# Kernel optimization log

Measured on AMD Instinct MI355X. Metric: run time of the kernel, lower is better.

## Reference

```python
import jax, jax.numpy as jnp
import numpy as np

# Spiking-neuron constants (ALIF_Neuron / output_Neuron are not in the given
# source; we use the standard surrogate-gradient spiking update from this repo
# family: mem = prev*decay*(1-spike) + input; spike = Heaviside(mem-thresh)).
THRESH = 0.5
LENS = 0.5
DECAY = 0.2

B, T, I, H = 64, 512, 256, 512

@jax.custom_vjp
def spike_fn(v):
    return (v > THRESH).astype(v.dtype)

def _spike_fwd(v):
    return spike_fn(v), v

def _spike_bwd(v, g):
    sg = (jnp.abs(v - THRESH) < LENS).astype(v.dtype) / (2.0 * LENS)
    return (g * sg,)

spike_fn.defvjp(_spike_fwd, _spike_bwd)


def setup_inputs() -> dict:
    key = jax.random.key(0)
    ks = jax.random.split(key, 7)
    sc = 0.05
    return {
        "x": jax.random.normal(ks[0], (B, T, I), jnp.float32),
        "Wx0": jax.random.normal(ks[1], (I, 4 * H), jnp.float32) * sc,
        "Wh0": jax.random.normal(ks[2], (H, 4 * H), jnp.float32) * sc,
        "bh0": jax.random.normal(ks[3], (4 * H,), jnp.float32) * sc,
        "Wx1": jax.random.normal(ks[4], (H, 4 * H), jnp.float32) * sc,
        "Wh1": jax.random.normal(ks[5], (H, 4 * H), jnp.float32) * sc,
        "bh1": jax.random.normal(ks[6], (4 * H,), jnp.float32) * sc,
    }


def _cell(xt, s, h, c, Wx, Wh, bh, is_output):
    # ifgo: [B, 4H]; chunk order i, f, g, o as in the torch code
    ifgo = xt @ Wx + h @ Wh + bh
    i, f, g, o = jnp.split(ifgo, 4, axis=-1)
    c_next = jax.nn.sigmoid(f) * c + jax.nn.sigmoid(i) * jnp.tanh(g)
    h_next = jax.nn.sigmoid(o) * jnp.tanh(c_next)
    if is_output:
        # output_Neuron(x, h_next): leaky integration of membrane with input
        h_next = h_next * DECAY + xt
        return s, h_next, c_next
    # ALIF_Neuron(s, h_next, s): adaptive mem update + surrogate spike
    mem = s * DECAY * (1.0 - s) + h_next
    s_new = spike_fn(mem)
    return s_new, mem, c_next


def reference(x, Wx0, Wh0, bh0, Wx1, Wh1, bh1):
    Bb = x.shape[0]
    z = jnp.zeros((Bb, H), x.dtype)
    init = (z, z, z, z, z, z)  # s0, h0, c0, s1, h1, c1

    def step(carry, xt):
        s0, h0, c0, s1, h1, c1 = carry
        s0, h0, c0 = _cell(xt, s0, h0, c0, Wx0, Wh0, bh0, False)
        # layer 1 consumes the spike output s0 of layer 0
        s1, h1, c1 = _cell(s0, s1, h1, c1, Wx1, Wh1, bh1, True)
        return (s0, h0, c0, s1, h1, c1), h1

    xs = jnp.swapaxes(x, 0, 1)  # [T, B, I]
    carry, outs = jax.lax.scan(step, init, xs)
    out = jnp.swapaxes(outs, 0, 1)  # [B, T, H] (batch_first)
    s0, h0, c0, s1, h1, c1 = carry
    s = jnp.stack([s0, s1])
    h = jnp.stack([h0, h1])
    c = jnp.stack([c0, c1])
    return out, s, h, c
```

## Files before the change

### kernel.cpp

```cpp
#include <hip/hip_runtime.h>
#include <math.h>

typedef float vf4 __attribute__((ext_vector_type(4)));

constexpr int T  = 512;
constexpr int BB = 64;
constexpr int II = 256;
constexpr int HH = 512;

constexpr int SOFF = BB * T * HH;
constexpr int HOFF = SOFF + 2 * BB * HH;
constexpr int COFF = HOFF + 2 * BB * HH;

constexpr int WS_WC0 = 0;
constexpr int WS_WC1 = 1572864;
constexpr int WS_BH0 = 3670016;
constexpr int WS_BH1 = 3672064;
constexpr int WS_HX0 = 3674112;
constexpr int WS_HX1 = 3739648;

__device__ __forceinline__ void bypass_st(float* p, float v) {
  asm volatile("global_store_dword %0, %1, off sc1" :: "v"(p), "v"(v) : "memory");
}
__device__ __forceinline__ void bypass_ld2x4(const vf4* p0, const vf4* p1, vf4& r0, vf4& r1) {
  asm volatile(
      "global_load_dwordx4 %0, %2, off sc1\n\t"
      "global_load_dwordx4 %1, %3, off sc1\n\t"
      "s_waitcnt vmcnt(0)"
      : "=&v"(r0), "=&v"(r1) : "v"(p0), "v"(p1) : "memory");
}

__device__ __forceinline__ bool tag_ok(float v, bool hi) {
  return hi ? (v > 6.0f) : (v > 2.0f && v < 6.0f);
}

__device__ __forceinline__ float sigf(float x) { return 1.0f / (1.0f + __expf(-x)); }
__device__ __forceinline__ float tanh_fast(float x) {
  return 1.0f - 2.0f / (1.0f + __expf(2.0f * x));
}

__device__ __forceinline__ float sxor(float v, int m) { return __shfl_xor(v, m, 64); }
__device__ __forceinline__ vf4 sxor4(vf4 v, int m) {
  vf4 r; r.x = sxor(v.x, m); r.y = sxor(v.y, m); r.z = sxor(v.z, m); r.w = sxor(v.w, m);
  return r;
}

__device__ __forceinline__ int rev3(int v) {
  return ((v & 1) << 2) | (v & 2) | ((v >> 2) & 1);
}

__device__ __forceinline__ vf4 reduce8(const vf4* acc, int kl) {
  const int sel = kl & 1;
  vf4 n0[4];
#pragma unroll
  for (int i = 0; i < 4; ++i) {
    vf4 snd = sel ? acc[i] : acc[i + 4];
    vf4 kp  = sel ? acc[i + 4] : acc[i];
    n0[i] = kp + sxor4(snd, 1);
  }
  const int sel2 = (kl >> 1) & 1;
  vf4 n1[2];
#pragma unroll
  for (int i = 0; i < 2; ++i) {
    vf4 snd = sel2 ? n0[i] : n0[i + 2];
    vf4 kp  = sel2 ? n0[i + 2] : n0[i];
    n1[i] = kp + sxor4(snd, 2);
  }
  const int sel3 = (kl >> 2) & 1;
  vf4 snd = sel3 ? n1[0] : n1[1];
  vf4 kp  = sel3 ? n1[1] : n1[0];
  vf4 r = kp + sxor4(snd, 4);
  r += sxor4(r, 8);
  r += sxor4(r, 16);
  r += sxor4(r, 32);
  return r;
}

__global__ void pack_wc(const float* __restrict__ A, const float* __restrict__ B,
                        int Ka, int K, float* __restrict__ Wp) {
  const int j = blockIdx.x;
  for (int k = threadIdx.x; k < K; k += 256) {
    const float* src = (k < Ka) ? (A + (size_t)k * 2048) : (B + (size_t)(k - Ka) * 2048);
    vf4 v = {src[j], src[512 + j], src[1024 + j], src[1536 + j]};
    ((vf4*)Wp)[(size_t)j * K + k] = v;
  }
}

__global__ void pack_bias(const float* __restrict__ bh0, const float* __restrict__ bh1,
                          float* __restrict__ bh0p, float* __restrict__ bh1p) {
  const int i = blockIdx.x * blockDim.x + threadIdx.x;
  if (i < 2048) {
    bh0p[i] = bh0[(i & 3) * 512 + (i >> 2)];
  } else {
    int q = i - 2048;
    bh1p[q] = bh1[(q & 3) * 512 + (q >> 2)];
  }
}

__global__ void fill_tag(float* __restrict__ p, float v) {
  p[blockIdx.x * 1024 + threadIdx.x] = v;
}

__global__ __launch_bounds__(1024, 4) void aslstm_main(
    const vf4* __restrict__ Wc0p, const vf4* __restrict__ Wc1p,
    const vf4* __restrict__ bh0p, const vf4* __restrict__ bh1p,
    const float* __restrict__ x,
    float* __restrict__ hx0, float* __restrict__ hx1,
    float* __restrict__ out) {
  const int wg  = blockIdx.x;
  const int xcd = wg & 7;
  const int a   = wg >> 3;
  const int g   = a & 7;
  const int s   = (a >> 3) * 8 + xcd;
  const int tid = threadIdx.x;
  const int jo  = tid >> 6;
  const int kl  = tid & 63;
  const int j   = s * 16 + jo;
  const int b_loc  = rev3(kl & 7);
  const int b_glob = g * 8 + b_loc;
  const bool rep0  = (kl < 8);

  __shared__ float cat0[2][8][776];
  __shared__ float cat1[2][8][1032];

  float c0 = 0.0f, c1 = 0.0f, sp = 0.0f;

  const int pl = (jo << 1) | (kl >> 5);
  const int lc = kl & 31;
  const int js = pl * 16 + (lc >> 1);
  const int b0 = (lc & 1) * 4;
  const int fo = g * 4096 + pl * 128 + lc * 4;

  vf4 w0r[3][4];
  {
    const vf4* wr = Wc0p + (size_t)j * 768;
#pragma unroll
    for (int ig = 0; ig < 3; ++ig) {
      const int k0 = ig * 256 + kl * 4;
#pragma unroll
      for (int q = 0; q < 4; ++q) w0r[ig][q] = wr[k0 + q];
    }
  }

  if (tid < 512) {
    int bx = tid >> 6, kx = (tid & 63) * 4;
    *(vf4*)&cat0[0][bx][kx] = *(const vf4*)&x[(size_t)(g * 8 + bx) * (T * II) + kx];
  }
  {
    int bz = tid >> 7, kz = (tid & 127) * 4;
    *(vf4*)&cat0[0][bz][256 + kz] = vf4{0.0f, 0.0f, 0.0f, 0.0f};
  }
  __syncthreads();

  for (int t = 0; t < T; ++t) {
    const int p0 = t & 1, p1 = p0 ^ 1;
    const bool tagm = ((t >> 1) & 1) != 0;
    const bool tagh = (((t + 3) >> 1) & 1) != 0;
    const float offm = tagm ? 8.0f : 4.0f;
    const float offh = tagh ? 8.0f : 4.0f;

    vf4 acc[8];
#pragma unroll
    for (int b = 0; b < 8; ++b) acc[b] = vf4{0, 0, 0, 0};
#pragma unroll
    for (int ig = 0; ig < 3; ++ig) {
      const int k0 = ig * 256 + kl * 4;
#pragma unroll
      for (int b = 0; b < 8; ++b) {
        vf4 av = *(const vf4*)&cat0[p0][b][k0];
        acc[b] += av.x * w0r[ig][0]; acc[b] += av.y * w0r[ig][1];
        acc[b] += av.z * w0r[ig][2]; acc[b] += av.w * w0r[ig][3];
      }
    }

    {
      vf4 p = reduce8(acc, kl) + bh0p[j];
      float cn  = sigf(p.y) * c0 + sigf(p.x) * tanh_fast(p.z);
      float mem = sigf(p.w) * tanh_fast(cn);
      float sn  = (mem > 0.5f) ? 1.0f : 0.0f;
      c0 = cn; sp = sn;
      if (rep0) {
        bypass_st(&hx0[p0 * 32768 + g * 4096 + j * 8 + b_loc], mem + offm);
        if (t == T - 1) {
          out[SOFF + b_glob * 512 + j] = sn;
          out[HOFF + b_glob * 512 + j] = mem;
          out[COFF + b_glob * 512 + j] = cn;
        }
      }
    }

    vf4 xv = vf4{0, 0, 0, 0};
    if (tid < 512 && t < T - 1) {
      int bx = tid >> 6, kx = (tid & 63) * 4;
      xv = *(const vf4*)&x[(size_t)(g * 8 + bx) * (T * II) + (size_t)(t + 1) * II + kx];
    }

    {
      const vf4* mp = (const vf4*)(hx0 + p0 * 32768 + fo);
      const vf4* hp = (const vf4*)(hx1 + p1 * 32768 + fo);
      vf4 mv, hv;
      int tries = 0;
      for (;;) {
        bypass_ld2x4(mp, hp, mv, hv);
        bool ok = tag_ok(mv.x, tagm) && tag_ok(mv.y, tagm) &&
                  tag_ok(mv.z, tagm) && tag_ok(mv.w, tagm) &&
                  tag_ok(hv.x, tagh) && tag_ok(hv.y, tagh) &&
                  tag_ok(hv.z, tagh) && tag_ok(hv.w, tagh);
        if (__all(ok)) break;
        if (++tries > 4) __builtin_amdgcn_s_sleep(1);
      }
      const vf4 om = {offm, offm, offm, offm};
      const vf4 oh = {offh, offh, offh, offh};
      vf4 mm = mv - om;
      vf4 hh = hv - oh;
      cat0[p1][b0 + 0][256 + js] = mm.x;
      cat0[p1][b0 + 1][256 + js] = mm.y;
      cat0[p1][b0 + 2][256 + js] = mm.z;
      cat0[p1][b0 + 3][256 + js] = mm.w;
      cat1[p0][b0 + 0][js] = (mm.x > 0.5f) ? 1.0f : 0.0f;
      cat1[p0][b0 + 1][js] = (mm.y > 0.5f) ? 1.0f : 0.0f;
      cat1[p0][b0 + 2][js] = (mm.z > 0.5f) ? 1.0f : 0.0f;
      cat1[p0][b0 + 3][js] = (mm.w > 0.5f) ? 1.0f : 0.0f;
      cat1[p0][b0 + 0][512 + js] = hh.x;
      cat1[p0][b0 + 1][512 + js] = hh.y;
      cat1[p0][b0 + 2][512 + js] = hh.z;
      cat1[p0][b0 + 3][512 + js] = hh.w;
      if (tid < 512) {
        int bx = tid >> 6, kx = (tid & 63) * 4;
        *(vf4*)&cat0[p1][bx][kx] = xv;
      }
    }
    __syncthreads();

#pragma unroll
    for (int b = 0; b < 8; ++b) acc[b] = vf4{0, 0, 0, 0};
    {
      const vf4* wr = Wc1p + (size_t)j * 1024;
#pragma unroll
      for (int ig = 0; ig < 4; ++ig) {
        const int k0 = ig * 256 + kl * 4;
        vf4 w0 = wr[k0], w1 = wr[k0 + 1], w2 = wr[k0 + 2], w3 = wr[k0 + 3];
#pragma unroll
        for (int b = 0; b < 8; ++b) {
          vf4 av = *(const vf4*)&cat1[p0][b][k0];
          acc[b] += av.x * w0; acc[b] += av.y * w1;
          acc[b] += av.z * w2; acc[b] += av.w * w3;
        }
      }
    }

    {
      vf4 p = reduce8(acc, kl) + bh1p[j];
      float cn  = sigf(p.y) * c1 + sigf(p.x) * tanh_fast(p.z);
      float hn  = sigf(p.w) * tanh_fast(cn);
      float h1n = hn * 0.2f + sp;
      c1 = cn;
      if (rep0) {
        bypass_st(&hx1[p0 * 32768 + g * 4096 + j * 8 + b_loc], h1n + offm);
        out[(size_t)b_glob * (T * HH) + (size_t)t * HH + j] = h1n;
        if (t == T - 1) {
          out[HOFF + 32768 + b_glob * 512 + j] = h1n;
          out[COFF + 32768 + b_glob * 512 + j] = cn;
        }
      }
    }
  }
}

extern "C" void kernel_launch(void* const* d_in, const int* in_sizes, int n_in,
                              void* d_out, int out_size, void* d_ws, size_t ws_size,
                              hipStream_t stream) {
  const float* x   = (const float*)d_in[0];
  const float* Wx0 = (const float*)d_in[1];
  const float* Wh0 = (const float*)d_in[2];
  const float* bh0 = (const float*)d_in[3];
  const float* Wx1 = (const float*)d_in[4];
  const float* Wh1 = (const float*)d_in[5];
  const float* bh1 = (const float*)d_in[6];
  float* out = (float*)d_out;
  float* ws  = (float*)d_ws;

  float* Wc0p  = ws + WS_WC0;
  float* Wc1p  = ws + WS_WC1;
  float* bh0pf = ws + WS_BH0;
  float* bh1pf = ws + WS_BH1;
  float* hx0   = ws + WS_HX0;
  float* hx1   = ws + WS_HX1;

  hipMemsetAsync(hx0, 0, 2 * 64 * 512 * sizeof(float), stream);
  hipMemsetAsync(hx1, 0, 64 * 512 * sizeof(float), stream);
  hipMemsetAsync(out + SOFF + BB * HH, 0, BB * HH * sizeof(float), stream);

  pack_wc<<<dim3(512), dim3(256), 0, stream>>>(Wx0, Wh0, 256, 768, Wc0p);
  pack_wc<<<dim3(512), dim3(256), 0, stream>>>(Wx1, Wh1, 512, 1024, Wc1p);
  pack_bias<<<dim3(16), dim3(256), 0, stream>>>(bh0, bh1, bh0pf, bh1pf);
  fill_tag<<<dim3(32), dim3(1024), 0, stream>>>(hx1 + 32768, 8.0f);

  aslstm_main<<<dim3(256), dim3(1024), 0, stream>>>(
      (const vf4*)Wc0p, (const vf4*)Wc1p, (const vf4*)bh0pf, (const vf4*)bh1pf,
      x, hx0, hx1, out);
}
```

Before: 7.482 ms.

## Split recurrent LSTM blocks to 8 hidden units and drop LDS double buffering

The persistent recurrent kernel now launches 512 workgroups of 512 threads instead of 256 of 1024, so each workgroup owns 8 hidden units. The cross-workgroup exchange is widened: each thread polls and loads two 16-byte chunks per buffer and writes them straight into a single-buffered LDS layout. The LDS double buffers are removed and an extra barrier is added before the exchange writes. The polling backoff also gains a longer sleep tier. The aim is smaller, cheaper per-block barriers and more even spread across CUs, at the cost of twice as many workgroups polling the global flags and one more barrier per step.

```diff
diff --git a/kernel.cpp b/kernel.cpp
--- a/kernel.cpp
+++ b/kernel.cpp
@@ -22,16 +22,23 @@
 __device__ __forceinline__ void bypass_st(float* p, float v) {
   asm volatile("global_store_dword %0, %1, off sc1" :: "v"(p), "v"(v) : "memory");
 }
-__device__ __forceinline__ void bypass_ld2x4(const vf4* p0, const vf4* p1, vf4& r0, vf4& r1) {
+__device__ __forceinline__ void bypass_ld4x4(const vf4* p0, const vf4* p1,
+                                             vf4& m0, vf4& m1, vf4& h0, vf4& h1) {
   asm volatile(
-      "global_load_dwordx4 %0, %2, off sc1\n\t"
-      "global_load_dwordx4 %1, %3, off sc1\n\t"
+      "global_load_dwordx4 %0, %4, off sc1\n\t"
+      "global_load_dwordx4 %1, %4, off offset:16 sc1\n\t"
+      "global_load_dwordx4 %2, %5, off sc1\n\t"
+      "global_load_dwordx4 %3, %5, off offset:16 sc1\n\t"
       "s_waitcnt vmcnt(0)"
-      : "=&v"(r0), "=&v"(r1) : "v"(p0), "v"(p1) : "memory");
+      : "=&v"(m0), "=&v"(m1), "=&v"(h0), "=&v"(h1)
+      : "v"(p0), "v"(p1) : "memory");
 }
 
 __device__ __forceinline__ bool tag_ok(float v, bool hi) {
   return hi ? (v > 6.0f) : (v > 2.0f && v < 6.0f);
+}
+__device__ __forceinline__ bool tag_ok4(vf4 v, bool hi) {
+  return tag_ok(v.x, hi) && tag_ok(v.y, hi) && tag_ok(v.z, hi) && tag_ok(v.w, hi);
 }
 
 __device__ __forceinline__ float sigf(float x) { return 1.0f / (1.0f + __expf(-x)); }
@@ -101,7 +108,7 @@
   p[blockIdx.x * 1024 + threadIdx.x] = v;
 }
 
-__global__ __launch_bounds__(1024, 4) void aslstm_main(
+__global__ __launch_bounds__(512, 4) void aslstm_main(
     const vf4* __restrict__ Wc0p, const vf4* __restrict__ Wc1p,
     const vf4* __restrict__ bh0p, const vf4* __restrict__ bh1p,
     const float* __restrict__ x,
@@ -115,21 +122,17 @@
   const int tid = threadIdx.x;
   const int jo  = tid >> 6;
   const int kl  = tid & 63;
-  const int j   = s * 16 + jo;
+  const int j   = s * 8 + jo;
   const int b_loc  = rev3(kl & 7);
   const int b_glob = g * 8 + b_loc;
   const bool rep0  = (kl < 8);
 
-  __shared__ float cat0[2][8][776];
-  __shared__ float cat1[2][8][1032];
+  __shared__ float cat0[8][776];
+  __shared__ float cat1[8][1032];
 
   float c0 = 0.0f, c1 = 0.0f, sp = 0.0f;
 
-  const int pl = (jo << 1) | (kl >> 5);
-  const int lc = kl & 31;
-  const int js = pl * 16 + (lc >> 1);
-  const int b0 = (lc & 1) * 4;
-  const int fo = g * 4096 + pl * 128 + lc * 4;
+  const int fo = g * 4096 + tid * 8;
 
   vf4 w0r[3][4];
   {
@@ -142,13 +145,12 @@
     }
   }
 
-  if (tid < 512) {
+  {
     int bx = tid >> 6, kx = (tid & 63) * 4;
-    *(vf4*)&cat0[0][bx][kx] = *(const vf4*)&x[(size_t)(g * 8 + bx) * (T * II) + kx];
-  }
-  {
-    int bz = tid >> 7, kz = (tid & 127) * 4;
-    *(vf4*)&cat0[0][bz][256 + kz] = vf4{0.0f, 0.0f, 0.0f, 0.0f};
+    *(vf4*)&cat0[bx][kx] = *(const vf4*)&x[(size_t)(g * 8 + bx) * (T * II) + kx];
+    int kz = (tid & 63) * 8;
+    *(vf4*)&cat0[bx][256 + kz] = vf4{0.0f, 0.0f, 0.0f, 0.0f};
+    *(vf4*)&cat0[bx][256 + kz + 4] = vf4{0.0f, 0.0f, 0.0f, 0.0f};
   }
   __syncthreads();
 
@@ -167,7 +169,7 @@
       const int k0 = ig * 256 + kl * 4;
 #pragma unroll
       for (int b = 0; b < 8; ++b) {
-        vf4 av = *(const vf4*)&cat0[p0][b][k0];
+        vf4 av = *(const vf4*)&cat0[b][k0];
         acc[b] += av.x * w0r[ig][0]; acc[b] += av.y * w0r[ig][1];
         acc[b] += av.z * w0r[ig][2]; acc[b] += av.w * w0r[ig][3];
       }
@@ -190,44 +192,51 @@
     }
 
     vf4 xv = vf4{0, 0, 0, 0};
-    if (tid < 512 && t < T - 1) {
+    if (t < T - 1) {
       int bx = tid >> 6, kx = (tid & 63) * 4;
       xv = *(const vf4*)&x[(size_t)(g * 8 + bx) * (T * II) + (size_t)(t + 1) * II + kx];
     }
+
+    __syncthreads();
 
     {
       const vf4* mp = (const vf4*)(hx0 + p0 * 32768 + fo);
       const vf4* hp = (const vf4*)(hx1 + p1 * 32768 + fo);
-      vf4 mv, hv;
+      vf4 m0, m1, h0v, h1v;
       int tries = 0;
       for (;;) {
-        bypass_ld2x4(mp, hp, mv, hv);
-        bool ok = tag_ok(mv.x, tagm) && tag_ok(mv.y, tagm) &&
-                  tag_ok(mv.z, tagm) && tag_ok(mv.w, tagm) &&
-                  tag_ok(hv.x, tagh) && tag_ok(hv.y, tagh) &&
-                  tag_ok(hv.z, tagh) && tag_ok(hv.w, tagh);
+        bypass_ld4x4(mp, hp, m0, m1, h0v, h1v);
+        bool ok = tag_ok4(m0, tagm) && tag_ok4(m1, tagm) &&
+                  tag_ok4(h0v, tagh) && tag_ok4(h1v, tagh);
         if (__all(ok)) break;
-        if (++tries > 4) __builtin_amdgcn_s_sleep(1);
+        ++tries;
+        if (tries > 16)     __builtin_amdgcn_s_sleep(4);
+        else if (tries > 4) __builtin_amdgcn_s_sleep(1);
       }
       const vf4 om = {offm, offm, offm, offm};
       const vf4 oh = {offh, offh, offh, offh};
-      vf4 mm = mv - om;
-      vf4 hh = hv - oh;
-      cat0[p1][b0 + 0][256 + js] = mm.x;
-      cat0[p1][b0 + 1][256 + js] = mm.y;
-      cat0[p1][b0 + 2][256 + js] = mm.z;
-      cat0[p1][b0 + 3][256 + js] = mm.w;
-      cat1[p0][b0 + 0][js] = (mm.x > 0.5f) ? 1.0f : 0.0f;
-      cat1[p0][b0 + 1][js] = (mm.y > 0.5f) ? 1.0f : 0.0f;
-      cat1[p0][b0 + 2][js] = (mm.z > 0.5f) ? 1.0f : 0.0f;
-      cat1[p0][b0 + 3][js] = (mm.w > 0.5f) ? 1.0f : 0.0f;
-      cat1[p0][b0 + 0][512 + js] = hh.x;
-      cat1[p0][b0 + 1][512 + js] = hh.y;
-      cat1[p0][b0 + 2][512 + js] = hh.z;
-      cat1[p0][b0 + 3][512 + js] = hh.w;
-      if (tid < 512) {
+      vf4 ma = m0 - om, mb = m1 - om;
+      vf4 ha = h0v - oh, hb = h1v - oh;
+      const int jc = tid;
+      cat0[0][256 + jc] = ma.x; cat0[1][256 + jc] = ma.y;
+      cat0[2][256 + jc] = ma.z; cat0[3][256 + jc] = ma.w;
+      cat0[4][256 + jc] = mb.x; cat0[5][256 + jc] = mb.y;
+      cat0[6][256 + jc] = mb.z; cat0[7][256 + jc] = mb.w;
+      cat1[0][jc] = (ma.x > 0.5f) ? 1.0f : 0.0f;
+      cat1[1][jc] = (ma.y > 0.5f) ? 1.0f : 0.0f;
+      cat1[2][jc] = (ma.z > 0.5f) ? 1.0f : 0.0f;
+      cat1[3][jc] = (ma.w > 0.5f) ? 1.0f : 0.0f;
+      cat1[4][jc] = (mb.x > 0.5f) ? 1.0f : 0.0f;
+      cat1[5][jc] = (mb.y > 0.5f) ? 1.0f : 0.0f;
+      cat1[6][jc] = (mb.z > 0.5f) ? 1.0f : 0.0f;
+      cat1[7][jc] = (mb.w > 0.5f) ? 1.0f : 0.0f;
+      cat1[0][512 + jc] = ha.x; cat1[1][512 + jc] = ha.y;
+      cat1[2][512 + jc] = ha.z; cat1[3][512 + jc] = ha.w;
+      cat1[4][512 + jc] = hb.x; cat1[5][512 + jc] = hb.y;
+      cat1[6][512 + jc] = hb.z; cat1[7][512 + jc] = hb.w;
+      {
         int bx = tid >> 6, kx = (tid & 63) * 4;
-        *(vf4*)&cat0[p1][bx][kx] = xv;
+        *(vf4*)&cat0[bx][kx] = xv;
       }
     }
     __syncthreads();
@@ -242,7 +251,7 @@
         vf4 w0 = wr[k0], w1 = wr[k0 + 1], w2 = wr[k0 + 2], w3 = wr[k0 + 3];
 #pragma unroll
         for (int b = 0; b < 8; ++b) {
-          vf4 av = *(const vf4*)&cat1[p0][b][k0];
+          vf4 av = *(const vf4*)&cat1[b][k0];
           acc[b] += av.x * w0; acc[b] += av.y * w1;
           acc[b] += av.z * w2; acc[b] += av.w * w3;
         }
@@ -296,7 +305,7 @@
   pack_bias<<<dim3(16), dim3(256), 0, stream>>>(bh0, bh1, bh0pf, bh1pf);
   fill_tag<<<dim3(32), dim3(1024), 0, stream>>>(hx1 + 32768, 8.0f);
 
-  aslstm_main<<<dim3(256), dim3(1024), 0, stream>>>(
+  aslstm_main<<<dim3(512), dim3(512), 0, stream>>>(
       (const vf4*)Wc0p, (const vf4*)Wc1p, (const vf4*)bh0pf, (const vf4*)bh1pf,
       x, hx0, hx1, out);
 }
```

Result: slower. 8.230 ms (+10.0%).
